# Performance work log

Measured on AMD Instinct MI355X. Metric: run time of the kernel, lower is better.

Reference implementation:

```python
import jax, jax.numpy as jnp
import numpy as np

HOP = 768
NCB = 14
DIM = 512
VOCAB = 1024
W_SCALE = 0.02  # keep conv stacks numerically tame


def conv1d(x, w, b, stride=1, padding=0):
    # x: [B,C,L], w: [O,I,K] (torch layout), b: [O]
    y = jax.lax.conv_general_dilated(
        x, w, window_strides=(stride,), padding=[(padding, padding)],
        dimension_numbers=('NCH', 'OIH', 'NCH'))
    return y + b[None, :, None]


def conv_transpose1d(x, w, b, stride, padding):
    # torch ConvTranspose1d weight layout: (in, out, k)
    k = w.shape[2]
    w2 = jnp.flip(jnp.transpose(w, (1, 0, 2)), axis=2)  # -> OIH
    y = jax.lax.conv_general_dilated(
        x, w2, window_strides=(1,),
        padding=[(k - 1 - padding, k - 1 - padding)],
        lhs_dilation=(stride,),
        dimension_numbers=('NCH', 'OIH', 'NCH'))
    return y + b[None, :, None]


def setup_inputs() -> dict:
    key = jax.random.key(0)
    ks = jax.random.split(key, 16)
    f = lambda k, shp, s=W_SCALE: jax.random.normal(k, shp, dtype=jnp.float32) * s
    B, T = 2, 98304  # T = 768 * 128
    return {
        'audio': jax.random.normal(ks[0], (B, 1, T), dtype=jnp.float32),
        'codebooks': jax.random.normal(ks[1], (NCB, VOCAB, DIM), dtype=jnp.float32),
        'ew1': f(ks[2], (256, 1, 7)), 'eb1': f(ks[3], (256,)),
        'ew2': f(ks[4], (512, 256, 5)), 'eb2': f(ks[5], (512,)),
        'ew3': f(ks[6], (NCB * DIM, 512, 3)), 'eb3': f(ks[7], (NCB * DIM,)),
        'dw1': f(ks[8], (NCB * DIM, 512, 5)), 'db1': f(ks[9], (512,)),
        'dw2': f(ks[10], (256, 512, 5)), 'db2': f(ks[11], (256,)),
        'dw3': f(ks[12], (1, 256, 7)), 'db3': f(ks[13], (1,)),
    }


def reference(audio, codebooks, ew1, eb1, ew2, eb2, ew3, eb3,
              dw1, db1, dw2, db2, dw3, db3):
    B = audio.shape[0]
    # ---- encoder ----
    h = jax.nn.relu(conv1d(audio, ew1, eb1, stride=1, padding=3))
    h = jax.nn.relu(conv1d(h, ew2, eb2, stride=HOP, padding=2))
    h = conv1d(h, ew3, eb3, stride=1, padding=1)          # [B, NCB*DIM, S]
    S = h.shape[-1]
    emb = h.reshape(B, NCB, DIM, S).transpose(0, 1, 3, 2)  # [B, NCB, S, DIM]
    # ---- VQ: per-codebook squared L2 distance + argmin (same argmin as cdist) ----
    d2 = (jnp.sum(emb * emb, axis=-1, keepdims=True)            # [B,NCB,S,1]
          - 2.0 * jnp.einsum('bksd,kvd->bksv', emb, codebooks)  # [B,NCB,S,V]
          + jnp.sum(codebooks * codebooks, axis=-1)[None, :, None, :])
    codes = jnp.argmin(d2, axis=-1)                        # [B, NCB, S] int
    # ---- decode: embedding lookup + transposed conv decoder ----
    q = codebooks[jnp.arange(NCB)[None, :, None], codes]   # [B, NCB, S, DIM]
    q = q.transpose(0, 1, 3, 2).reshape(B, NCB * DIM, S)   # [B, NCB*DIM, S]
    a = jax.nn.relu(conv_transpose1d(q, dw1, db1, stride=HOP, padding=2))
    a = jax.nn.relu(conv1d(a, dw2, db2, stride=1, padding=2))
    a = jnp.tanh(conv1d(a, dw3, db3, stride=1, padding=3))
    return a  # [B, 1, (S-1)*HOP + 1]
```

## Files before the change

### kernel.cpp

```cpp
#include <hip/hip_runtime.h>
#include <hip/hip_bf16.h>
#include <math.h>

#define T_IN 98304
#define SS 128
#define NBATCH 2
#define NN 256
#define C1 256
#define C2 512
#define C3 7168
#define NCBK 14
#define DIMV 512
#define VOC 1024
#define TOUT 97537
#define HOP 768

#define OFF_CBN    0L
#define OFF_AB1    14336L
#define OFF_AB2    14848L
#define OFF_CCONST 15104L
#define OFF_H2C    15120L
#define OFF_H2XH   146192L
#define OFF_H2XL   342800L
#define OFF_H3H    539408L
#define OFF_H3L    1456912L
#define OFF_SCORES 2374416L
#define OFF_X1H    2374416L
#define OFF_X1L    2538256L
#define OFF_DW1T   539408L
#define OFF_XH     539408L
#define OFF_XL     3488528L
#define OFF_CODES  9714448L
#define OFF_QBF    9718032L
#define OFF_A1RAW  10635536L
#define OFF_DW2PH  10635536L
#define OFF_DW2PL  10963216L
#define OFF_A2ACT  11290896L
#define OFF_CBPH   11880720L
#define OFF_CBPL   15550736L
#define OFF_EW3PH  19220752L
#define OFF_EW3PL  24725776L
#define OFF_EW2PH  30230800L
#define OFF_EW2PL  30558480L

typedef __attribute__((ext_vector_type(8))) short short8;
typedef __attribute__((ext_vector_type(4))) float f32x4;

static __device__ inline ushort f2bf(float x) {
  __hip_bfloat16 h = __float2bfloat16(x);
  return *reinterpret_cast<ushort*>(&h);
}

static __device__ inline void split8(const float4 x0, const float4 x1,
                                     short8& h, short8& l) {
  float xs[8] = {x0.x, x0.y, x0.z, x0.w, x1.x, x1.y, x1.z, x1.w};
  #pragma unroll
  for (int e = 0; e < 8; ++e) {
    uint b = __float_as_uint(xs[e]);
    h[e] = (short)(b >> 16);
    float r = xs[e] - __uint_as_float(b & 0xffff0000u);
    l[e] = (short)(__float_as_uint(r) >> 16);
  }
}

__global__ void k_cbn(const float* __restrict__ cb, float* __restrict__ cbn) {
  int row = blockIdx.x * 4 + (threadIdx.x >> 6);
  int lane = threadIdx.x & 63;
  const float* p = cb + (long)row * DIMV;
  float s = 0.f;
  for (int d = lane; d < DIMV; d += 64) { float x = p[d]; s += x * x; }
  for (int off = 32; off; off >>= 1) s += __shfl_down(s, off);
  if (lane == 0) cbn[row] = s;
}

__global__ __launch_bounds__(256) void k_cbp(const float* __restrict__ cb,
    ushort* __restrict__ ph, ushort* __restrict__ pl) {
  int o8 = blockIdx.x * 256 + threadIdx.x;
  const int total = NCBK * VOC * DIMV / 8;
  if (o8 >= total) return;
  int frag = o8 >> 6, lane = o8 & 63;
  int quad = lane >> 4, l15 = lane & 15;
  int zmt = frag >> 4, kt = frag & 15;
  int row = zmt * 16 + l15;
  int k = kt * 32 + quad * 8;
  const float* s = cb + (long)row * DIMV + k;
  float4 x0 = *(const float4*)s;
  float4 x1 = *(const float4*)(s + 4);
  short8 h, l;
  split8(x0, x1, h, l);
  long off = (long)o8 * 8;
  *(short8*)(ph + off) = h;
  *(short8*)(pl + off) = l;
}

__global__ __launch_bounds__(256) void k_prep_ab2(const float* __restrict__ db1,
    const float* __restrict__ dw2, const float* __restrict__ db2,
    float* __restrict__ ab1, float* __restrict__ ab2) {
  __shared__ float red[256];
  int o = blockIdx.x, t = threadIdx.x;
  if (o == 0) { ab1[t] = fmaxf(db1[t], 0.f); ab1[t + 256] = fmaxf(db1[t + 256], 0.f); }
  const float* wp = dw2 + (long)o * C2 * 5;
  float acc = 0.f;
  #pragma unroll
  for (int h = 0; h < 2; ++h) {
    int c = t + h * 256;
    const float* p = wp + c * 5;
    float wsum = p[0] + p[1] + p[2] + p[3] + p[4];
    acc = fmaf(wsum, fmaxf(db1[c], 0.f), acc);
  }
  red[t] = acc;
  __syncthreads();
  for (int off = 128; off; off >>= 1) {
    if (t < off) red[t] += red[t + off];
    __syncthreads();
  }
  if (t == 0) ab2[o] = fmaxf(red[0] + db2[o], 0.f);
}

__global__ __launch_bounds__(256) void k_prep_c(const float* __restrict__ dw3,
    const float* __restrict__ db3, const float* __restrict__ ab2,
    float* __restrict__ cconst) {
  __shared__ float red[256];
  int t = threadIdx.x;
  float wsum3 = 0.f;
  #pragma unroll
  for (int j = 0; j < 7; ++j) wsum3 += dw3[t*7+j];
  red[t] = wsum3 * ab2[t];
  __syncthreads();
  for (int off = 128; off; off >>= 1) {
    if (t < off) red[t] += red[t + off];
    __syncthreads();
  }
  if (t == 0) cconst[0] = tanhf(red[0] + db3[0]);
}

__global__ __launch_bounds__(256) void k_enc1(const float* __restrict__ audio,
    const float* __restrict__ ew1, const float* __restrict__ eb1,
    ushort* __restrict__ X1h, ushort* __restrict__ X1l) {
  int n = blockIdx.x, ic = threadIdx.x;
  int b = n >> 7, s = n & 127;
  const float* ap = audio + (long)b * T_IN;
  int base = HOP * s - 5;
  float a[11];
  #pragma unroll
  for (int w = 0; w < 11; ++w) {
    int ai = base + w;
    a[w] = (ai >= 0 && ai < T_IN) ? ap[ai] : 0.f;
  }
  float w1[7];
  #pragma unroll
  for (int j = 0; j < 7; ++j) w1[j] = ew1[ic*7+j];
  float b1 = eb1[ic];
  #pragma unroll
  for (int jj = 0; jj < 5; ++jj) {
    int tcol = HOP * s + jj - 2;
    float v = 0.f;
    if (tcol >= 0) {
      float acc = b1;
      #pragma unroll
      for (int j = 0; j < 7; ++j) acc = fmaf(w1[j], a[jj + j], acc);
      v = fmaxf(acc, 0.f);
    }
    int k = ic * 5 + jj;
    int kt = k >> 5;
    int lane2 = ((k >> 3) & 3) * 16 + (n & 15);
    long idx = ((long)((n >> 4) * 40 + kt)) * 512 + lane2 * 8 + (k & 7);
    uint bi = __float_as_uint(v);
    X1h[idx] = (ushort)(bi >> 16);
    float r = v - __uint_as_float(bi & 0xffff0000u);
    X1l[idx] = (ushort)(__float_as_uint(r) >> 16);
  }
}

__global__ __launch_bounds__(256) void k_ew2p(const float* __restrict__ ew2,
    ushort* __restrict__ ph, ushort* __restrict__ pl) {
  int o8 = blockIdx.x * 256 + threadIdx.x;
  const int total = 512 * 1280 / 8;
  if (o8 >= total) return;
  int frag = o8 >> 6, lane = o8 & 63;
  int quad = lane >> 4, l15 = lane & 15;
  int mt = frag / 40, kt = frag - mt * 40;
  int m = mt * 16 + l15;
  int k = kt * 32 + quad * 8;
  const float* s = ew2 + (long)m * 1280 + k;
  float4 x0 = *(const float4*)s;
  float4 x1 = *(const float4*)(s + 4);
  short8 h, l;
  split8(x0, x1, h, l);
  long off = (long)o8 * 8;
  *(short8*)(ph + off) = h;
  *(short8*)(pl + off) = l;
}

__global__ __launch_bounds__(256) void gemm_enc2(const ushort* __restrict__ aH,
    const ushort* __restrict__ aL, const ushort* __restrict__ bH,
    const ushort* __restrict__ bL, const float* __restrict__ eb2,
    float* __restrict__ h2c) {
  __shared__ __align__(16) float red[4 * 2048];
  const int tid = threadIdx.x;
  const int w = tid >> 6, lane = tid & 63;
  const int l15 = lane & 15, quad = lane >> 4;
  const int m0 = blockIdx.x * 32, n0 = blockIdx.y * 64;
  const int mt0 = blockIdx.x * 2, nt0 = blockIdx.y * 4;
  const int kt0 = w * 10;
  f32x4 acc[2][4] = {};
  const ushort* aHB = aH + ((long)(mt0 * 40 + kt0)) * 512 + lane * 8;
  const ushort* aLB = aL + ((long)(mt0 * 40 + kt0)) * 512 + lane * 8;
  const ushort* bHB = bH + ((long)(nt0 * 40 + kt0)) * 512 + lane * 8;
  const ushort* bLB = bL + ((long)(nt0 * 40 + kt0)) * 512 + lane * 8;
  for (int kt = 0; kt < 10; ++kt) {
    short8 ah[2], al[2], bh[4], bl[4];
    #pragma unroll
    for (int i = 0; i < 2; ++i) {
      long o = ((long)(i * 40 + kt)) * 512;
      ah[i] = *(const short8*)(aHB + o);
      al[i] = *(const short8*)(aLB + o);
    }
    #pragma unroll
    for (int f = 0; f < 4; ++f) {
      long o = ((long)(f * 40 + kt)) * 512;
      bh[f] = *(const short8*)(bHB + o);
      bl[f] = *(const short8*)(bLB + o);
    }
    #pragma unroll
    for (int i = 0; i < 2; ++i)
      #pragma unroll
      for (int j = 0; j < 4; ++j) {
        acc[i][j] = __builtin_amdgcn_mfma_f32_16x16x32_bf16(ah[i], bh[j], acc[i][j], 0, 0, 0);
        acc[i][j] = __builtin_amdgcn_mfma_f32_16x16x32_bf16(ah[i], bl[j], acc[i][j], 0, 0, 0);
        acc[i][j] = __builtin_amdgcn_mfma_f32_16x16x32_bf16(al[i], bh[j], acc[i][j], 0, 0, 0);
      }
  }
  #pragma unroll
  for (int i = 0; i < 2; ++i)
    #pragma unroll
    for (int j = 0; j < 4; ++j)
      *(float4*)&red[w * 2048 + (i * 4 + j) * 256 + lane * 4] = *(float4*)&acc[i][j];
  __syncthreads();
  #pragma unroll
  for (int q = 0; q < 2; ++q) {
    const int c = 2 * w + q;
    const int i = c >> 2, j = c & 3;
    float4 s = make_float4(0.f, 0.f, 0.f, 0.f);
    #pragma unroll
    for (int g = 0; g < 4; ++g) {
      float4 t4 = *(const float4*)&red[g * 2048 + c * 256 + lane * 4];
      s.x += t4.x; s.y += t4.y; s.z += t4.z; s.w += t4.w;
    }
    const int obase = m0 + i * 16 + quad * 4;
    float4 bias = *(const float4*)(eb2 + obase);
    const int n = n0 + j * 16 + l15;
    float4 out;
    out.x = fmaxf(s.x + bias.x, 0.f);
    out.y = fmaxf(s.y + bias.y, 0.f);
    out.z = fmaxf(s.z + bias.z, 0.f);
    out.w = fmaxf(s.w + bias.w, 0.f);
    *(float4*)(h2c + (long)n * C2 + obase) = out;
  }
}

__global__ void k_h2x(const float* __restrict__ h2c, ushort* __restrict__ h2xph,
                      ushort* __restrict__ h2xpl) {
  int idx = blockIdx.x * 256 + threadIdx.x;
  const int total = NN * 1536;
  for (; idx < total; idx += gridDim.x * 256) {
    int grp = idx >> 9;
    int r = idx & 511;
    int e = r & 7, lane = r >> 3;
    int quad = lane >> 4, l15 = lane & 15;
    int nt = grp / 48, kt = grp - nt * 48;
    int n = nt * 16 + l15;
    int k = kt * 32 + quad * 8 + e;
    int ic = k / 3, j = k - ic * 3;
    int s2 = (n & 127) + j - 1;
    int b = n >> 7;
    float v = (s2 >= 0 && s2 < SS) ? h2c[(long)(b*SS + s2)*C2 + ic] : 0.f;
    uint bi = __float_as_uint(v);
    h2xph[idx] = (ushort)(bi >> 16);
    float rr = v - __uint_as_float(bi & 0xffff0000u);
    h2xpl[idx] = (ushort)(__float_as_uint(rr) >> 16);
  }
}

__global__ __launch_bounds__(256) void k_ew3p(const float* __restrict__ ew3,
    ushort* __restrict__ ph, ushort* __restrict__ pl) {
  int o8 = blockIdx.x * 256 + threadIdx.x;
  const int total = C3 * 1536 / 8;
  if (o8 >= total) return;
  int frag = o8 >> 6, lane = o8 & 63;
  int quad = lane >> 4, l15 = lane & 15;
  int mtL = frag / 48, kt = frag - mtL * 48;
  int m = mtL * 16 + l15;
  int k = kt * 32 + quad * 8;
  const float* s = ew3 + (long)m * 1536 + k;
  float4 x0 = *(const float4*)s;
  float4 x1 = *(const float4*)(s + 4);
  short8 h, l;
  split8(x0, x1, h, l);
  long off = (long)o8 * 8;
  *(short8*)(ph + off) = h;
  *(short8*)(pl + off) = l;
}

__global__ __launch_bounds__(256) void gemm_h3(const ushort* __restrict__ aH,
    const ushort* __restrict__ aL, const ushort* __restrict__ bH,
    const ushort* __restrict__ bL, const float* __restrict__ eb3,
    ushort* __restrict__ h3ph, ushort* __restrict__ h3pl) {
  __shared__ __align__(16) float red[4 * 4096];
  const int tid = threadIdx.x;
  const int w = tid >> 6, lane = tid & 63;
  const int l15 = lane & 15, quad = lane >> 4;
  const int bid = blockIdx.x;
  const int xcd = bid & 7, q = bid >> 3;
  const int mchunk = xcd * 14 + (q >> 2);
  const int nchunk = q & 3;
  const int mtL0 = mchunk * 4, nt0 = nchunk * 4, n0 = nchunk * 64;
  const int kt0 = w * 12;
  f32x4 acc[4][4] = {};
  const ushort* aHB = aH + ((long)(mtL0 * 48 + kt0)) * 512 + lane * 8;
  const ushort* aLB = aL + ((long)(mtL0 * 48 + kt0)) * 512 + lane * 8;
  const ushort* bHB = bH + ((long)(nt0 * 48 + kt0)) * 512 + lane * 8;
  const ushort* bLB = bL + ((long)(nt0 * 48 + kt0)) * 512 + lane * 8;
  for (int kt = 0; kt < 12; ++kt) {
    short8 ah[4], al[4], bh[4], bl[4];
    #pragma unroll
    for (int f = 0; f < 4; ++f) {
      long o = ((long)(f * 48 + kt)) * 512;
      ah[f] = *(const short8*)(aHB + o);
      al[f] = *(const short8*)(aLB + o);
      bh[f] = *(const short8*)(bHB + o);
      bl[f] = *(const short8*)(bLB + o);
    }
    #pragma unroll
    for (int i = 0; i < 4; ++i)
      #pragma unroll
      for (int j = 0; j < 4; ++j) {
        acc[i][j] = __builtin_amdgcn_mfma_f32_16x16x32_bf16(ah[i], bh[j], acc[i][j], 0, 0, 0);
        acc[i][j] = __builtin_amdgcn_mfma_f32_16x16x32_bf16(ah[i], bl[j], acc[i][j], 0, 0, 0);
        acc[i][j] = __builtin_amdgcn_mfma_f32_16x16x32_bf16(al[i], bh[j], acc[i][j], 0, 0, 0);
      }
  }
  #pragma unroll
  for (int i = 0; i < 4; ++i)
    #pragma unroll
    for (int j = 0; j < 4; ++j)
      *(float4*)&red[w * 4096 + (i * 4 + j) * 256 + lane * 4] = *(float4*)&acc[i][j];
  __syncthreads();
  const int mg0 = mchunk * 64 + w * 16 + quad * 4;
  float4 bias = *(const float4*)(eb3 + mg0);
  const int ktS = mg0 >> 5, quadk = (mg0 >> 3) & 3, es = mg0 & 7;
  #pragma unroll
  for (int j = 0; j < 4; ++j) {
    float4 s = *(const float4*)&red[(w * 4 + j) * 256 + lane * 4];
    #pragma unroll
    for (int r = 1; r < 4; ++r) {
      float4 tt = *(const float4*)&red[r * 4096 + (w * 4 + j) * 256 + lane * 4];
      s.x += tt.x; s.y += tt.y; s.z += tt.z; s.w += tt.w;
    }
    const int n = n0 + j * 16 + l15;
    float v0 = s.x + bias.x;
    float v1 = s.y + bias.y;
    float v2 = s.z + bias.z;
    float v3 = s.w + bias.w;
    uint b0 = __float_as_uint(v0), b1 = __float_as_uint(v1);
    uint b2 = __float_as_uint(v2), b3 = __float_as_uint(v3);
    uint2 hp;
    hp.x = (b0 >> 16) | (b1 & 0xffff0000u);
    hp.y = (b2 >> 16) | (b3 & 0xffff0000u);
    float r0 = v0 - __uint_as_float(b0 & 0xffff0000u);
    float r1 = v1 - __uint_as_float(b1 & 0xffff0000u);
    float r2 = v2 - __uint_as_float(b2 & 0xffff0000u);
    float r3 = v3 - __uint_as_float(b3 & 0xffff0000u);
    uint2 lp;
    lp.x = (__float_as_uint(r0) >> 16) | (__float_as_uint(r1) & 0xffff0000u);
    lp.y = (__float_as_uint(r2) >> 16) | (__float_as_uint(r3) & 0xffff0000u);
    long off = ((long)((n >> 4) * 224 + ktS)) * 512 + (quadk * 16 + (n & 15)) * 8 + es;
    *(uint2*)(h3ph + off) = hp;
    *(uint2*)(h3pl + off) = lp;
  }
}

__global__ __launch_bounds__(256) void gemm_scores(const ushort* __restrict__ aH,
    const ushort* __restrict__ aL, const ushort* __restrict__ bH,
    const ushort* __restrict__ bL, const float* __restrict__ cbn,
    float* __restrict__ scores) {
  __shared__ __align__(16) float red[4 * 4096];
  const int tid = threadIdx.x;
  const int w = tid >> 6, lane = tid & 63;
  const int l15 = lane & 15, quad = lane >> 4;
  const int m0 = blockIdx.x * 64, n0 = blockIdx.y * 64, z = blockIdx.z;
  const int mt0 = blockIdx.x * 4;
  const int kt0 = w * 4;
  f32x4 acc[4][4] = {};
  const ushort* aHB = aH + ((long)((z * 64 + mt0) * 16 + kt0)) * 512 + lane * 8;
  const ushort* aLB = aL + ((long)((z * 64 + mt0) * 16 + kt0)) * 512 + lane * 8;
  const ushort* bHB = bH + ((long)((n0 >> 4) * 224 + z * 16 + kt0)) * 512 + lane * 8;
  const ushort* bLB = bL + ((long)((n0 >> 4) * 224 + z * 16 + kt0)) * 512 + lane * 8;
  for (int kt = 0; kt < 4; ++kt) {
    short8 ah[4], al[4], bh[4], bl[4];
    #pragma unroll
    for (int f = 0; f < 4; ++f) {
      long oa = ((long)(f * 16 + kt)) * 512;
      long ob = ((long)(f * 224 + kt)) * 512;
      ah[f] = *(const short8*)(aHB + oa);
      al[f] = *(const short8*)(aLB + oa);
      bh[f] = *(const short8*)(bHB + ob);
      bl[f] = *(const short8*)(bLB + ob);
    }
    #pragma unroll
    for (int i = 0; i < 4; ++i)
      #pragma unroll
      for (int j = 0; j < 4; ++j) {
        acc[i][j] = __builtin_amdgcn_mfma_f32_16x16x32_bf16(ah[i], bh[j], acc[i][j], 0, 0, 0);
        acc[i][j] = __builtin_amdgcn_mfma_f32_16x16x32_bf16(ah[i], bl[j], acc[i][j], 0, 0, 0);
        acc[i][j] = __builtin_amdgcn_mfma_f32_16x16x32_bf16(al[i], bh[j], acc[i][j], 0, 0, 0);
      }
  }
  #pragma unroll
  for (int i = 0; i < 4; ++i)
    #pragma unroll
    for (int j = 0; j < 4; ++j)
      *(float4*)&red[w * 4096 + (i * 4 + j) * 256 + lane * 4] = *(float4*)&acc[i][j];
  __syncthreads();
  const int vbase = m0 + w * 16 + quad * 4;
  float4 cn = *(const float4*)(cbn + z * VOC + vbase);
  #pragma unroll
  for (int j = 0; j < 4; ++j) {
    float4 s = *(const float4*)&red[(w * 4 + j) * 256 + lane * 4];
    #pragma unroll
    for (int r = 1; r < 4; ++r) {
      float4 tt = *(const float4*)&red[r * 4096 + (w * 4 + j) * 256 + lane * 4];
      s.x += tt.x; s.y += tt.y; s.z += tt.z; s.w += tt.w;
    }
    const int n = n0 + j * 16 + l15;
    float4 out;
    out.x = cn.x - 2.f * s.x;
    out.y = cn.y - 2.f * s.y;
    out.z = cn.z - 2.f * s.z;
    out.w = cn.w - 2.f * s.w;
    *(float4*)(scores + ((long)z * NN + n) * VOC + vbase) = out;
  }
}

__global__ void k_argmin(const float* __restrict__ scores, int* __restrict__ codes) {
  int row = blockIdx.x;
  int lane = threadIdx.x;
  const float* p = scores + (long)row * VOC;
  float best = 3.4e38f; int bi = 0;
  for (int i = 0; i < 16; ++i) {
    int v = i * 64 + lane;
    float x = p[v];
    if (x < best) { best = x; bi = v; }
  }
  for (int off = 32; off; off >>= 1) {
    float ob = __shfl_down(best, off);
    int oi = __shfl_down(bi, off);
    if (ob < best || (ob == best && oi < bi)) { best = ob; bi = oi; }
  }
  if (lane == 0) codes[row] = bi;
}

__global__ __launch_bounds__(256) void k_dw1t(const float* __restrict__ dw1,
                                              ushort* __restrict__ dw1p) {
  __shared__ __align__(16) ushort T[64 * 72];
  int t = threadIdx.x;
  int k0 = blockIdx.x * 64, m0 = blockIdx.y * 64;
  int kk = t >> 2, mj = (t & 3) * 16;
  const float* src = dw1 + (long)(k0 + kk) * 2560 + m0 + mj;
  float x[16];
  *(float4*)&x[0]  = *(const float4*)(src);
  *(float4*)&x[4]  = *(const float4*)(src + 4);
  *(float4*)&x[8]  = *(const float4*)(src + 8);
  *(float4*)&x[12] = *(const float4*)(src + 12);
  #pragma unroll
  for (int l = 0; l < 16; ++l)
    T[(mj + l) * 72 + kk] = f2bf(x[l]);
  __syncthreads();
  int mo = t >> 2, kc = (t & 3) * 16;
  const int m = m0 + mo;
  const int mt = m >> 4, l15 = m & 15;
  #pragma unroll
  for (int h = 0; h < 2; ++h) {
    const int kk0 = kc + h * 8;
    const int kglob = k0 + kk0;
    const int kt = kglob >> 5;
    const int quad = (kglob >> 3) & 3;
    uint4 u = *(const uint4*)&T[mo * 72 + kk0];
    *(uint4*)(dw1p + ((long)(mt * 224 + kt)) * 512 + (quad * 16 + l15) * 8) = u;
  }
}

__global__ void k_gather_qbf(const float* __restrict__ cb, const int* __restrict__ codes,
                             ushort* __restrict__ qp) {
  int o = blockIdx.x * 256 + threadIdx.x;
  const int total = NN * C3 / 8;
  if (o >= total) return;
  int frag = o >> 6, r = o & 63;
  int quad = r >> 4, l15 = r & 15;
  int nt = frag / 224, kt = frag - nt * 224;
  int n = nt * 16 + l15;
  int kglob = kt * 32 + quad * 8;
  int kcb = kglob >> 9, d0 = kglob & 511;
  int code = codes[kcb * NN + n];
  const float* s = cb + ((long)(kcb * VOC + code)) * DIMV + d0;
  float4 x0 = *(const float4*)s;
  float4 x1 = *(const float4*)(s + 4);
  uint4 u;
  u.x = (uint)f2bf(x0.x) | ((uint)f2bf(x0.y) << 16);
  u.y = (uint)f2bf(x0.z) | ((uint)f2bf(x0.w) << 16);
  u.z = (uint)f2bf(x1.x) | ((uint)f2bf(x1.y) << 16);
  u.w = (uint)f2bf(x1.z) | ((uint)f2bf(x1.w) << 16);
  ((uint4*)qp)[o] = u;
}

__global__ __launch_bounds__(1024) void gemm_a1_mfma(const ushort* __restrict__ dw1p,
    const ushort* __restrict__ qp, float* __restrict__ a1raw) {
  __shared__ __align__(16) float red[4 * 4096];
  const int tid = threadIdx.x;
  const int w = tid >> 6, lane = tid & 63;
  const int l15 = lane & 15, quad = lane >> 4;
  const int mt0 = blockIdx.x * 4, nt0 = blockIdx.y * 4;
  const int kt0 = w * 14;
  f32x4 acc[4][4] = {};
  const ushort* aB = dw1p + ((long)(mt0 * 224 + kt0)) * 512 + lane * 8;
  const ushort* bB = qp   + ((long)(nt0 * 224 + kt0)) * 512 + lane * 8;
  #pragma unroll 2
  for (int kt = 0; kt < 14; ++kt) {
    short8 ah[4], bh[4];
    #pragma unroll
    for (int f = 0; f < 4; ++f) {
      ah[f] = *(const short8*)(aB + ((long)(f * 224 + kt)) * 512);
      bh[f] = *(const short8*)(bB + ((long)(f * 224 + kt)) * 512);
    }
    #pragma unroll
    for (int i = 0; i < 4; ++i)
      #pragma unroll
      for (int j = 0; j < 4; ++j)
        acc[i][j] = __builtin_amdgcn_mfma_f32_16x16x32_bf16(ah[i], bh[j], acc[i][j], 0, 0, 0);
  }
  float4 rsum = make_float4(0.f, 0.f, 0.f, 0.f);
  #pragma unroll
  for (int r = 0; r < 4; ++r) {
    if ((w >> 2) == r) {
      #pragma unroll
      for (int i = 0; i < 4; ++i)
        #pragma unroll
        for (int j = 0; j < 4; ++j)
          *(float4*)&red[(w & 3) * 4096 + (i * 4 + j) * 256 + lane * 4] = *(float4*)&acc[i][j];
    }
    __syncthreads();
    #pragma unroll
    for (int g = 0; g < 4; ++g) {
      float4 t4 = *(const float4*)&red[g * 4096 + w * 256 + lane * 4];
      rsum.x += t4.x; rsum.y += t4.y; rsum.z += t4.z; rsum.w += t4.w;
    }
    __syncthreads();
  }
  const int ci = w >> 2, cj = w & 3;
  const int n = nt0 * 16 + cj * 16 + l15;
  const int mb = mt0 * 16 + ci * 16 + quad * 4;
  float v[4] = {rsum.x, rsum.y, rsum.z, rsum.w};
  #pragma unroll
  for (int reg = 0; reg < 4; ++reg) {
    int m = mb + reg;
    int c = m / 5, jj = m - c * 5;
    a1raw[((long)(n * 5 + jj)) * C2 + c] = v[reg];
  }
}

__global__ void k_x2(const float* __restrict__ a1raw, const float* __restrict__ ab1g,
                     const float* __restrict__ db1, ushort* __restrict__ Xh,
                     ushort* __restrict__ Xl) {
  int idx = blockIdx.x * 256 + threadIdx.x;
  const int total = 2304 * 2560;
  for (; idx < total; idx += gridDim.x * 256) {
    int grp = idx >> 9;
    int r = idx & 511;
    int e = r & 7, lane = r >> 3;
    int quad = lane >> 4, l15 = lane & 15;
    int nt = grp / 80, kt = grp - nt * 80;
    int nu = nt * 16 + l15;
    int ck = kt * 32 + quad * 8 + e;
    int n = nu / 9, u = nu - n * 9;
    int c = ck / 5, jj = ck - c * 5;
    int w = u + jj;
    int s = n & 127;
    int tc = HOP * s - 6 + w;
    float v;
    if (tc < 0 || tc > TOUT - 1) v = 0.f;
    else if (w >= 4 && w <= 8)
      v = fmaxf(db1[c] + a1raw[((long)(n * 5 + (w - 4))) * C2 + c], 0.f);
    else v = ab1g[c];
    uint bi = __float_as_uint(v);
    Xh[idx] = (ushort)(bi >> 16);
    float rr = v - __uint_as_float(bi & 0xffff0000u);
    Xl[idx] = (ushort)(__float_as_uint(rr) >> 16);
  }
}

__global__ __launch_bounds__(256) void k_dw2p(const float* __restrict__ dw2,
    ushort* __restrict__ ph, ushort* __restrict__ pl) {
  int o8 = blockIdx.x * 256 + threadIdx.x;
  const int total = 256 * 2560 / 8;
  if (o8 >= total) return;
  int frag = o8 >> 6, lane = o8 & 63;
  int quad = lane >> 4, l15 = lane & 15;
  int mt = frag / 80, kt = frag - mt * 80;
  int m = mt * 16 + l15;
  int k = kt * 32 + quad * 8;
  const float* s = dw2 + (long)m * 2560 + k;
  float4 x0 = *(const float4*)s;
  float4 x1 = *(const float4*)(s + 4);
  short8 h, l;
  split8(x0, x1, h, l);
  long off = (long)o8 * 8;
  *(short8*)(ph + off) = h;
  *(short8*)(pl + off) = l;
}

__global__ __launch_bounds__(256) void gemm_dec2(const ushort* __restrict__ aH,
    const ushort* __restrict__ aL, const ushort* __restrict__ bH,
    const ushort* __restrict__ bL, const float* __restrict__ db2,
    float* __restrict__ a2act) {
  __shared__ __align__(16) float red[4 * 4096];
  const int tid = threadIdx.x;
  const int w = tid >> 6, lane = tid & 63;
  const int l15 = lane & 15, quad = lane >> 4;
  const int mt0 = blockIdx.x * 4, nt0 = blockIdx.y * 4;
  const int m0 = mt0 * 16, n0 = nt0 * 16;
  const int kt0 = w * 20;
  f32x4 acc[4][4] = {};
  const ushort* aHB = aH + ((long)(mt0 * 80 + kt0)) * 512 + lane * 8;
  const ushort* aLB = aL + ((long)(mt0 * 80 + kt0)) * 512 + lane * 8;
  const ushort* bHB = bH + ((long)(nt0 * 80 + kt0)) * 512 + lane * 8;
  const ushort* bLB = bL + ((long)(nt0 * 80 + kt0)) * 512 + lane * 8;
  for (int kt = 0; kt < 20; ++kt) {
    short8 ah[4], al[4], bh[4], bl[4];
    #pragma unroll
    for (int f = 0; f < 4; ++f) {
      long o = ((long)(f * 80 + kt)) * 512;
      ah[f] = *(const short8*)(aHB + o);
      al[f] = *(const short8*)(aLB + o);
      bh[f] = *(const short8*)(bHB + o);
      bl[f] = *(const short8*)(bLB + o);
    }
    #pragma unroll
    for (int i = 0; i < 4; ++i)
      #pragma unroll
      for (int j = 0; j < 4; ++j) {
        acc[i][j] = __builtin_amdgcn_mfma_f32_16x16x32_bf16(ah[i], bh[j], acc[i][j], 0, 0, 0);
        acc[i][j] = __builtin_amdgcn_mfma_f32_16x16x32_bf16(ah[i], bl[j], acc[i][j], 0, 0, 0);
        acc[i][j] = __builtin_amdgcn_mfma_f32_16x16x32_bf16(al[i], bh[j], acc[i][j], 0, 0, 0);
      }
  }
  #pragma unroll
  for (int i = 0; i < 4; ++i)
    #pragma unroll
    for (int j = 0; j < 4; ++j)
      *(float4*)&red[w * 4096 + (i * 4 + j) * 256 + lane * 4] = *(float4*)&acc[i][j];
  __syncthreads();
  const int mb = m0 + w * 16 + quad * 4;
  float4 bias = *(const float4*)(db2 + mb);
  #pragma unroll
  for (int j = 0; j < 4; ++j) {
    float4 s = *(const float4*)&red[(w * 4 + j) * 256 + lane * 4];
    #pragma unroll
    for (int r = 1; r < 4; ++r) {
      float4 tt = *(const float4*)&red[r * 4096 + (w * 4 + j) * 256 + lane * 4];
      s.x += tt.x; s.y += tt.y; s.z += tt.z; s.w += tt.w;
    }
    const int nu = n0 + j * 16 + l15;
    float4 out;
    out.x = fmaxf(s.x + bias.x, 0.f);
    out.y = fmaxf(s.y + bias.y, 0.f);
    out.z = fmaxf(s.z + bias.z, 0.f);
    out.w = fmaxf(s.w + bias.w, 0.f);
    *(float4*)(a2act + (long)nu * C1 + mb) = out;
  }
}

__global__ void k_fill(float* __restrict__ outp, const float* __restrict__ cconst) {
  float v = cconst[0];
  int idx = blockIdx.x * 256 + threadIdx.x;
  const int total = NBATCH * TOUT;
  for (; idx < total; idx += gridDim.x * 256) outp[idx] = v;
}

__global__ __launch_bounds__(256) void k_dec3(const float* __restrict__ a2act,
    const float* __restrict__ ab2g, const float* __restrict__ dw3,
    const float* __restrict__ db3, float* __restrict__ outp) {
  __shared__ float sa2[9 * C1];
  __shared__ float sb[C1];
  int n = blockIdx.x;
  int s = n & 127, b = n >> 7;
  int t = threadIdx.x;
  for (int i = t; i < 9 * C1; i += 256) sa2[i] = a2act[(long)n * 9 * C1 + i];
  sb[t] = ab2g[t];
  __syncthreads();
  int wv = t >> 6, lane = t & 63;
  float b3 = db3[0];
  for (int w15 = wv; w15 < 15; w15 += 4) {
    int tc = HOP * s - 7 + w15;
    if (tc < 0 || tc > TOUT - 1) continue;
    float part = 0.f;
    for (int cc = lane; cc < C1; cc += 64) {
      #pragma unroll
      for (int j = 0; j < 7; ++j) {
        int wcol = tc + j - 3;
        float x;
        if (wcol < 0 || wcol > TOUT - 1) x = 0.f;
        else {
          int du = wcol - (HOP * s - 4);
          x = (du >= 0 && du <= 8) ? sa2[du * C1 + cc] : sb[cc];
        }
        part = fmaf(dw3[cc*7+j], x, part);
      }
    }
    for (int off = 32; off; off >>= 1) part += __shfl_down(part, off);
    if (lane == 0) outp[(long)b * TOUT + tc] = tanhf(part + b3);
  }
}

extern "C" void kernel_launch(void* const* d_in, const int* in_sizes, int n_in,
                              void* d_out, int out_size, void* d_ws, size_t ws_size,
                              hipStream_t stream) {
  const float* audio = (const float*)d_in[0];
  const float* cb    = (const float*)d_in[1];
  const float* ew1   = (const float*)d_in[2];
  const float* eb1   = (const float*)d_in[3];
  const float* ew2   = (const float*)d_in[4];
  const float* eb2   = (const float*)d_in[5];
  const float* ew3   = (const float*)d_in[6];
  const float* eb3   = (const float*)d_in[7];
  const float* dw1   = (const float*)d_in[8];
  const float* db1   = (const float*)d_in[9];
  const float* dw2   = (const float*)d_in[10];
  const float* db2   = (const float*)d_in[11];
  const float* dw3   = (const float*)d_in[12];
  const float* db3   = (const float*)d_in[13];
  float* outp = (float*)d_out;
  float* ws = (float*)d_ws;

  float*  cbn    = ws + OFF_CBN;
  float*  ab1    = ws + OFF_AB1;
  float*  ab2    = ws + OFF_AB2;
  float*  cconst = ws + OFF_CCONST;
  float*  h2c    = ws + OFF_H2C;
  ushort* h2xph  = (ushort*)(ws + OFF_H2XH);
  ushort* h2xpl  = (ushort*)(ws + OFF_H2XL);
  ushort* h3ph   = (ushort*)(ws + OFF_H3H);
  ushort* h3pl   = (ushort*)(ws + OFF_H3L);
  float*  scores = ws + OFF_SCORES;
  ushort* X1h    = (ushort*)(ws + OFF_X1H);
  ushort* X1l    = (ushort*)(ws + OFF_X1L);
  ushort* cbph   = (ushort*)(ws + OFF_CBPH);
  ushort* cbpl   = (ushort*)(ws + OFF_CBPL);
  ushort* ew3ph  = (ushort*)(ws + OFF_EW3PH);
  ushort* ew3pl  = (ushort*)(ws + OFF_EW3PL);
  ushort* ew2ph  = (ushort*)(ws + OFF_EW2PH);
  ushort* ew2pl  = (ushort*)(ws + OFF_EW2PL);
  ushort* dw1p   = (ushort*)(ws + OFF_DW1T);
  ushort* Xh     = (ushort*)(ws + OFF_XH);
  ushort* Xl     = (ushort*)(ws + OFF_XL);
  int*    codes  = (int*)(ws + OFF_CODES);
  ushort* qp     = (ushort*)(ws + OFF_QBF);
  float*  a1raw  = ws + OFF_A1RAW;
  ushort* dw2ph  = (ushort*)(ws + OFF_DW2PH);
  ushort* dw2pl  = (ushort*)(ws + OFF_DW2PL);
  float*  a2act  = ws + OFF_A2ACT;

  k_cbn<<<3584, 256, 0, stream>>>(cb, cbn);
  k_cbp<<<3584, 256, 0, stream>>>(cb, cbph, cbpl);
  k_prep_ab2<<<C1, 256, 0, stream>>>(db1, dw2, db2, ab1, ab2);
  k_prep_c<<<1, 256, 0, stream>>>(dw3, db3, ab2, cconst);
  k_enc1<<<NN, 256, 0, stream>>>(audio, ew1, eb1, X1h, X1l);
  k_ew2p<<<320, 256, 0, stream>>>(ew2, ew2ph, ew2pl);
  gemm_enc2<<<dim3(16, 4), 256, 0, stream>>>(ew2ph, ew2pl, X1h, X1l, eb2, h2c);
  k_h2x<<<384, 256, 0, stream>>>(h2c, h2xph, h2xpl);
  k_ew3p<<<5376, 256, 0, stream>>>(ew3, ew3ph, ew3pl);
  gemm_h3<<<448, 256, 0, stream>>>(ew3ph, ew3pl, h2xph, h2xpl, eb3, h3ph, h3pl);
  gemm_scores<<<dim3(16, 4, 14), 256, 0, stream>>>(cbph, cbpl, h3ph, h3pl, cbn, scores);
  k_argmin<<<NCBK * NN, 64, 0, stream>>>(scores, codes);
  k_dw1t<<<dim3(112, 40), 256, 0, stream>>>(dw1, dw1p);
  k_gather_qbf<<<896, 256, 0, stream>>>(cb, codes, qp);
  gemm_a1_mfma<<<dim3(40, 4), 1024, 0, stream>>>(dw1p, qp, a1raw);
  k_x2<<<4096, 256, 0, stream>>>(a1raw, ab1, db1, Xh, Xl);
  k_dw2p<<<320, 256, 0, stream>>>(dw2, dw2ph, dw2pl);
  gemm_dec2<<<dim3(4, 36), 256, 0, stream>>>(dw2ph, dw2pl, Xh, Xl, db2, a2act);
  k_fill<<<256, 256, 0, stream>>>(outp, cconst);
  k_dec3<<<NN, 256, 0, stream>>>(a2act, ab2, dw3, db3, outp);
}
```

Baseline: 394.1 us.

## Fuse argmin into scores GEMM epilogue and codebook norm into packing

The scores GEMM no longer writes the full 14x256x1024 distance matrix. Each block instead reduces its 64-column tile to a per-row partial minimum and index, and a small second kernel combines the 16 partials per row. Separately, the codebook norm computation is folded into the codebook bf16 hi/lo packing kernel so the codebook is read once. This removes a large scores round trip through memory and one launch, at the cost of extra shuffles and shared-memory reductions in the GEMM epilogue.

Result: no change. 389.3 us (-1.2%).

```diff
diff --git a/kernel.cpp b/kernel.cpp
--- a/kernel.cpp
+++ b/kernel.cpp
@@ -24,7 +24,6 @@
 #define OFF_H2XL   342800L
 #define OFF_H3H    539408L
 #define OFF_H3L    1456912L
-#define OFF_SCORES 2374416L
 #define OFF_X1H    2374416L
 #define OFF_X1L    2538256L
 #define OFF_DW1T   539408L
@@ -42,6 +41,8 @@
 #define OFF_EW3PL  24725776L
 #define OFF_EW2PH  30230800L
 #define OFF_EW2PL  30558480L
+#define OFF_PVAL   30886160L
+#define OFF_PIDX   30943504L
 
 typedef __attribute__((ext_vector_type(8))) short short8;
 typedef __attribute__((ext_vector_type(4))) float f32x4;
@@ -63,34 +64,38 @@
   }
 }
 
-__global__ void k_cbn(const float* __restrict__ cb, float* __restrict__ cbn) {
-  int row = blockIdx.x * 4 + (threadIdx.x >> 6);
-  int lane = threadIdx.x & 63;
-  const float* p = cb + (long)row * DIMV;
-  float s = 0.f;
-  for (int d = lane; d < DIMV; d += 64) { float x = p[d]; s += x * x; }
-  for (int off = 32; off; off >>= 1) s += __shfl_down(s, off);
-  if (lane == 0) cbn[row] = s;
-}
-
 __global__ __launch_bounds__(256) void k_cbp(const float* __restrict__ cb,
-    ushort* __restrict__ ph, ushort* __restrict__ pl) {
-  int o8 = blockIdx.x * 256 + threadIdx.x;
-  const int total = NCBK * VOC * DIMV / 8;
-  if (o8 >= total) return;
-  int frag = o8 >> 6, lane = o8 & 63;
+    ushort* __restrict__ ph, ushort* __restrict__ pl, float* __restrict__ cbn) {
+  __shared__ float red[256];
+  int zmt = blockIdx.x;
+  int t = threadIdx.x;
+  int lane = t & 63, fg = t >> 6;
   int quad = lane >> 4, l15 = lane & 15;
-  int zmt = frag >> 4, kt = frag & 15;
   int row = zmt * 16 + l15;
-  int k = kt * 32 + quad * 8;
-  const float* s = cb + (long)row * DIMV + k;
-  float4 x0 = *(const float4*)s;
-  float4 x1 = *(const float4*)(s + 4);
-  short8 h, l;
-  split8(x0, x1, h, l);
-  long off = (long)o8 * 8;
-  *(short8*)(ph + off) = h;
-  *(short8*)(pl + off) = l;
+  float ss = 0.f;
+  #pragma unroll
+  for (int h = 0; h < 4; ++h) {
+    int kt = fg * 4 + h;
+    int k = kt * 32 + quad * 8;
+    const float* s = cb + (long)row * DIMV + k;
+    float4 x0 = *(const float4*)s;
+    float4 x1 = *(const float4*)(s + 4);
+    short8 hh, ll;
+    split8(x0, x1, hh, ll);
+    long off = ((long)zmt * 16 + kt) * 512 + lane * 8;
+    *(short8*)(ph + off) = hh;
+    *(short8*)(pl + off) = ll;
+    ss += x0.x*x0.x + x0.y*x0.y + x0.z*x0.z + x0.w*x0.w
+        + x1.x*x1.x + x1.y*x1.y + x1.z*x1.z + x1.w*x1.w;
+  }
+  red[t] = ss;
+  __syncthreads();
+  if (t < 16) {
+    float s = 0.f;
+    #pragma unroll
+    for (int g = 0; g < 16; ++g) s += red[t + g * 16];
+    cbn[zmt * 16 + t] = s;
+  }
 }
 
 __global__ __launch_bounds__(256) void k_prep_ab2(const float* __restrict__ db1,
@@ -383,8 +388,10 @@
 __global__ __launch_bounds__(256) void gemm_scores(const ushort* __restrict__ aH,
     const ushort* __restrict__ aL, const ushort* __restrict__ bH,
     const ushort* __restrict__ bL, const float* __restrict__ cbn,
-    float* __restrict__ scores) {
+    float* __restrict__ pval, int* __restrict__ pidx) {
   __shared__ __align__(16) float red[4 * 4096];
+  __shared__ float wv_[4 * 64];
+  __shared__ int   wi_[4 * 64];
   const int tid = threadIdx.x;
   const int w = tid >> 6, lane = tid & 63;
   const int l15 = lane & 15, quad = lane >> 4;
@@ -432,32 +439,49 @@
       float4 tt = *(const float4*)&red[r * 4096 + (w * 4 + j) * 256 + lane * 4];
       s.x += tt.x; s.y += tt.y; s.z += tt.z; s.w += tt.w;
     }
-    const int n = n0 + j * 16 + l15;
-    float4 out;
-    out.x = cn.x - 2.f * s.x;
-    out.y = cn.y - 2.f * s.y;
-    out.z = cn.z - 2.f * s.z;
-    out.w = cn.w - 2.f * s.w;
-    *(float4*)(scores + ((long)z * NN + n) * VOC + vbase) = out;
-  }
-}
-
-__global__ void k_argmin(const float* __restrict__ scores, int* __restrict__ codes) {
-  int row = blockIdx.x;
-  int lane = threadIdx.x;
-  const float* p = scores + (long)row * VOC;
-  float best = 3.4e38f; int bi = 0;
-  for (int i = 0; i < 16; ++i) {
-    int v = i * 64 + lane;
-    float x = p[v];
-    if (x < best) { best = x; bi = v; }
-  }
-  for (int off = 32; off; off >>= 1) {
-    float ob = __shfl_down(best, off);
-    int oi = __shfl_down(bi, off);
-    if (ob < best || (ob == best && oi < bi)) { best = ob; bi = oi; }
-  }
-  if (lane == 0) codes[row] = bi;
+    float o0 = cn.x - 2.f * s.x;
+    float o1 = cn.y - 2.f * s.y;
+    float o2 = cn.z - 2.f * s.z;
+    float o3 = cn.w - 2.f * s.w;
+    float bv = o0; int bm = vbase;
+    if (o1 < bv) { bv = o1; bm = vbase + 1; }
+    if (o2 < bv) { bv = o2; bm = vbase + 2; }
+    if (o3 < bv) { bv = o3; bm = vbase + 3; }
+    #pragma unroll
+    for (int off = 16; off <= 32; off <<= 1) {
+      float ov = __shfl_xor(bv, off);
+      int om = __shfl_xor(bm, off);
+      if (ov < bv || (ov == bv && om < bm)) { bv = ov; bm = om; }
+    }
+    if (quad == 0) { wv_[w * 64 + j * 16 + l15] = bv; wi_[w * 64 + j * 16 + l15] = bm; }
+  }
+  __syncthreads();
+  if (tid < 64) {
+    float bv = wv_[tid]; int bm = wi_[tid];
+    #pragma unroll
+    for (int g = 1; g < 4; ++g) {
+      float ov = wv_[g * 64 + tid]; int om = wi_[g * 64 + tid];
+      if (ov < bv || (ov == bv && om < bm)) { bv = ov; bm = om; }
+    }
+    long prow = (long)z * NN + n0 + tid;
+    pval[prow * 16 + blockIdx.x] = bv;
+    pidx[prow * 16 + blockIdx.x] = bm;
+  }
+}
+
+__global__ void k_argmin2(const float* __restrict__ pval, const int* __restrict__ pidx,
+                          int* __restrict__ codes) {
+  int row = blockIdx.x * 256 + threadIdx.x;
+  if (row >= NCBK * NN) return;
+  const float* pv = pval + (long)row * 16;
+  const int*   pi = pidx + (long)row * 16;
+  float bv = pv[0]; int bm = pi[0];
+  #pragma unroll
+  for (int c = 1; c < 16; ++c) {
+    float v = pv[c]; int m = pi[c];
+    if (v < bv || (v == bv && m < bm)) { bv = v; bm = m; }
+  }
+  codes[row] = bm;
 }
 
 __global__ __launch_bounds__(256) void k_dw1t(const float* __restrict__ dw1,
@@ -750,7 +774,6 @@
   ushort* h2xpl  = (ushort*)(ws + OFF_H2XL);
   ushort* h3ph   = (ushort*)(ws + OFF_H3H);
   ushort* h3pl   = (ushort*)(ws + OFF_H3L);
-  float*  scores = ws + OFF_SCORES;
   ushort* X1h    = (ushort*)(ws + OFF_X1H);
   ushort* X1l    = (ushort*)(ws + OFF_X1L);
   ushort* cbph   = (ushort*)(ws + OFF_CBPH);
@@ -759,6 +782,8 @@
   ushort* ew3pl  = (ushort*)(ws + OFF_EW3PL);
   ushort* ew2ph  = (ushort*)(ws + OFF_EW2PH);
   ushort* ew2pl  = (ushort*)(ws + OFF_EW2PL);
+  float*  pval   = ws + OFF_PVAL;
+  int*    pidx   = (int*)(ws + OFF_PIDX);
   ushort* dw1p   = (ushort*)(ws + OFF_DW1T);
   ushort* Xh     = (ushort*)(ws + OFF_XH);
   ushort* Xl     = (ushort*)(ws + OFF_XL);
@@ -769,8 +794,7 @@
   ushort* dw2pl  = (ushort*)(ws + OFF_DW2PL);
   float*  a2act  = ws + OFF_A2ACT;
 
-  k_cbn<<<3584, 256, 0, stream>>>(cb, cbn);
-  k_cbp<<<3584, 256, 0, stream>>>(cb, cbph, cbpl);
+  k_cbp<<<896, 256, 0, stream>>>(cb, cbph, cbpl, cbn);
   k_prep_ab2<<<C1, 256, 0, stream>>>(db1, dw2, db2, ab1, ab2);
   k_prep_c<<<1, 256, 0, stream>>>(dw3, db3, ab2, cconst);
   k_enc1<<<NN, 256, 0, stream>>>(audio, ew1, eb1, X1h, X1l);
@@ -779,8 +803,8 @@
   k_h2x<<<384, 256, 0, stream>>>(h2c, h2xph, h2xpl);
   k_ew3p<<<5376, 256, 0, stream>>>(ew3, ew3ph, ew3pl);
   gemm_h3<<<448, 256, 0, stream>>>(ew3ph, ew3pl, h2xph, h2xpl, eb3, h3ph, h3pl);
-  gemm_scores<<<dim3(16, 4, 14), 256, 0, stream>>>(cbph, cbpl, h3ph, h3pl, cbn, scores);
-  k_argmin<<<NCBK * NN, 64, 0, stream>>>(scores, codes);
+  gemm_scores<<<dim3(16, 4, 14), 256, 0, stream>>>(cbph, cbpl, h3ph, h3pl, cbn, pval, pidx);
+  k_argmin2<<<14, 256, 0, stream>>>(pval, pidx, codes);
   k_dw1t<<<dim3(112, 40), 256, 0, stream>>>(dw1, dw1p);
   k_gather_qbf<<<896, 256, 0, stream>>>(cb, codes, qp);
   gemm_a1_mfma<<<dim3(40, 4), 1024, 0, stream>>>(dw1p, qp, a1raw);
```
